# Kernel optimization log

Measured on AMD Instinct MI355X. Metric: run time of the kernel, lower is better.

Reference implementation:

```python
import jax, jax.numpy as jnp
import numpy as np

WIN = (8, 7, 7)
N_TOK = WIN[0] * WIN[1] * WIN[2]  # 392
DIM = 128
N_HEADS = 4
TABLE = (2 * WIN[0] - 1) * (2 * WIN[1] - 1) * (2 * WIN[2] - 1)  # 2535


def _relative_position_index():
    # Faithful port of the torch buffer construction in __init__.
    coords = np.stack(np.meshgrid(np.arange(WIN[0]), np.arange(WIN[1]), np.arange(WIN[2]), indexing='ij'))
    flat = coords.reshape(3, -1)                       # (3, N)
    rel = flat[:, :, None] - flat[:, None, :]          # (3, N, N)
    rel = rel.transpose(1, 2, 0).astype(np.int64)      # (N, N, 3)
    rel[..., 0] += WIN[0] - 1
    rel[..., 1] += WIN[1] - 1
    rel[..., 2] += WIN[2] - 1
    rel[..., 0] *= (2 * WIN[1] - 1) * (2 * WIN[2] - 1)
    rel[..., 1] *= 2 * WIN[2] - 1
    return rel.sum(-1)                                 # (N, N)


def setup_inputs() -> dict:
    key = jax.random.key(0)
    k1, k2, k3, k4 = jax.random.split(key, 4)
    B_ = 256   # B=1 batch * 256 windows of a 32x224x224 clip (D=32,H=56,W=56)
    nW = 256
    x = jax.random.normal(k1, (B_, N_TOK, DIM), dtype=jnp.float32)
    mask = jnp.zeros((nW, N_TOK, N_TOK), dtype=jnp.float32)  # 0/-inf shift mask; non-shift -> zeros
    bias_table = 0.02 * jax.random.normal(k2, (TABLE, N_HEADS), dtype=jnp.float32)
    rel_index = jnp.asarray(_relative_position_index(), dtype=jnp.int32)
    qkv_w = 0.02 * jax.random.normal(k3, (3 * DIM, DIM), dtype=jnp.float32)
    proj_w = 0.02 * jax.random.normal(k4, (DIM, DIM), dtype=jnp.float32)
    proj_b = jnp.zeros((DIM,), dtype=jnp.float32)
    return {"x": x, "mask": mask, "bias_table": bias_table, "rel_index": rel_index,
            "qkv_w": qkv_w, "proj_w": proj_w, "proj_b": proj_b}


def reference(x, mask, bias_table, rel_index, qkv_w, proj_w, proj_b):
    B_, N, C = x.shape
    nH = N_HEADS
    hd = C // nH
    scale = hd ** -0.5
    # qkv projection (no bias), split heads -> (3, B_, nH, N, hd)
    qkv = (x @ qkv_w.T).reshape(B_, N, 3, nH, hd).transpose(2, 0, 3, 1, 4)
    q, k, v = qkv[0], qkv[1], qkv[2]
    # relative position bias: gather table -> (nH, N, N)
    bias = bias_table[rel_index.reshape(-1)].reshape(N, N, nH).transpose(2, 0, 1)
    # scores: (B_, nH, N, N)
    attn = jnp.einsum('bhnd,bhmd->bhnm', q * scale, k) + bias[None]
    nW = mask.shape[0]
    attn = attn.reshape(B_ // nW, nW, nH, N, N) + mask[None, :, None]
    attn = jax.nn.softmax(attn.reshape(B_, nH, N, N), axis=-1)
    y = jnp.einsum('bhnm,bhmd->bhnd', attn, v)            # (B_, nH, N, hd)
    y = y.transpose(0, 2, 1, 3).reshape(B_, N, C)
    return y @ proj_w.T + proj_b
```

## Files before the change

### kernel.cpp

```cpp
#include <hip/hip_runtime.h>
#include <hip/hip_bf16.h>
#include <stdint.h>

#define NTOK 392
#define DIM  128
#define NH   4
#define HD   32
#define NCH  13
#define KST  36
#define VST  396
#define L2E  1.44269504f
#define BPQ  416

typedef __attribute__((ext_vector_type(4))) float f32x4;
typedef __attribute__((ext_vector_type(4))) short s16x4;
typedef __attribute__((ext_vector_type(8))) short s16x8;

union Frag { s16x8 v; struct { s16x4 lo, hi; } h; };
union PF { s16x8 v; uint32_t u[4]; };

__device__ __forceinline__ short f2bf(float f) {
  union { float f; uint32_t u; } v; v.f = f;
  uint32_t r = v.u + 0x7fffu + ((v.u >> 16) & 1u);
  return (short)(r >> 16);
}
__device__ __forceinline__ s16x4 cvt4(f32x4 a) {
  s16x4 r; r.x = f2bf(a.x); r.y = f2bf(a.y); r.z = f2bf(a.z); r.w = f2bf(a.w);
  return r;
}
__device__ __forceinline__ float fexp2(float x) {
  float r; asm("v_exp_f32 %0, %1" : "=v"(r) : "v"(x)); return r;
}
__device__ __forceinline__ void bb2f(s16x8 b, f32x4& lo, f32x4& hi) {
  union { s16x8 s; uint32_t u[4]; } x; x.s = b;
  union { uint32_t u; float f; } t;
  t.u = x.u[0] << 16;          lo.x = t.f;
  t.u = x.u[0] & 0xffff0000u;  lo.y = t.f;
  t.u = x.u[1] << 16;          lo.z = t.f;
  t.u = x.u[1] & 0xffff0000u;  lo.w = t.f;
  t.u = x.u[2] << 16;          hi.x = t.f;
  t.u = x.u[2] & 0xffff0000u;  hi.y = t.f;
  t.u = x.u[3] << 16;          hi.z = t.f;
  t.u = x.u[3] & 0xffff0000u;  hi.w = t.f;
}

__device__ __forceinline__ void sm_pv(f32x4 s0, f32x4 s1,
                                      f32x4& o0, f32x4& o1,
                                      float& mrun, float& nmrl, float& lrun,
                                      const Frag& vf0, const Frag& vf1) {
  float cm = fmaxf(fmaxf(fmaxf(s0.x, s0.y), fmaxf(s0.z, s0.w)),
                   fmaxf(fmaxf(s1.x, s1.y), fmaxf(s1.z, s1.w)));
  if (__any(cm > mrun + 8.f)) {
    float tmx = fmaxf(cm, __shfl_xor(cm, 16));
    tmx = fmaxf(tmx, __shfl_xor(tmx, 32));
    const float mnew = fmaxf(mrun, tmx);
    const float al = fexp2((mrun - mnew) * L2E);
    #pragma unroll
    for (int rr = 0; rr < 4; ++rr) { o0[rr] *= al; o1[rr] *= al; }
    lrun *= al; mrun = mnew; nmrl = -mnew * L2E;
  }
  float p0 = fexp2(fmaf(s0.x, L2E, nmrl));
  float p1 = fexp2(fmaf(s0.y, L2E, nmrl));
  float p2 = fexp2(fmaf(s0.z, L2E, nmrl));
  float p3 = fexp2(fmaf(s0.w, L2E, nmrl));
  float p4 = fexp2(fmaf(s1.x, L2E, nmrl));
  float p5 = fexp2(fmaf(s1.y, L2E, nmrl));
  float p6 = fexp2(fmaf(s1.z, L2E, nmrl));
  float p7 = fexp2(fmaf(s1.w, L2E, nmrl));
  lrun += ((p0 + p1) + (p2 + p3)) + ((p4 + p5) + (p6 + p7));
  PF pf;
  asm("v_cvt_pk_bf16_f32 %0, %1, %2" : "=v"(pf.u[0]) : "v"(p0), "v"(p1));
  asm("v_cvt_pk_bf16_f32 %0, %1, %2" : "=v"(pf.u[1]) : "v"(p2), "v"(p3));
  asm("v_cvt_pk_bf16_f32 %0, %1, %2" : "=v"(pf.u[2]) : "v"(p4), "v"(p5));
  asm("v_cvt_pk_bf16_f32 %0, %1, %2" : "=v"(pf.u[3]) : "v"(p6), "v"(p7));
  o0 = __builtin_amdgcn_mfma_f32_16x16x32_bf16(vf0.v, pf.v, o0, 0, 0, 0);
  o1 = __builtin_amdgcn_mfma_f32_16x16x32_bf16(vf1.v, pf.v, o1, 0, 0, 0);
}

__global__ void k_biasperm(const float* __restrict__ bt, const int* __restrict__ ri,
                           short* __restrict__ bias_perm) {
  int i = blockIdx.x * 256 + threadIdx.x;
  if (i >= NH * NTOK * BPQ) return;
  int h = i / (NTOK * BPQ);
  int r = i - h * (NTOK * BPQ);
  int q = r / BPQ;
  int p = r - q * BPQ;
  int c = p >> 5, w2 = p & 31;
  int g = w2 >> 3, hb = (w2 >> 2) & 1, jj = w2 & 3;
  int kv = c * 32 + hb * 16 + g * 4 + jj;
  float v = -3e30f;
  if (kv < NTOK) v = bt[ri[q * NTOK + kv] * NH + h];
  bias_perm[i] = f2bf(v);
}

__global__ void k_wprep(const float* __restrict__ qkvw, const float* __restrict__ pw,
                        short* __restrict__ wq_bf, short* __restrict__ wp_bf) {
  int i = blockIdx.x * 256 + threadIdx.x;
  if (i < 3 * DIM * DIM) wq_bf[i] = f2bf(qkvw[i]);
  if (i < DIM * DIM)     wp_bf[i] = f2bf(pw[i]);
}

__global__ __launch_bounds__(256, 2)
void k_qkv(const float* __restrict__ x, const short* __restrict__ wq_bf,
           short* __restrict__ q_ws, short* __restrict__ k_ws,
           short* __restrict__ v_ws) {
  __shared__ short xs[64 * 136];
  __shared__ short wl[128 * 136];
  const int t  = threadIdx.x;
  const int m0 = blockIdx.x * 64;
  {
    const int r = t >> 2, c0 = (t & 3) * 32;
    const float* src = x + (size_t)(m0 + r) * DIM + c0;
    short* dst = xs + r * 136 + c0;
    #pragma unroll
    for (int i = 0; i < 8; ++i)
      *(s16x4*)(dst + 4*i) = cvt4(*(const f32x4*)(src + 4*i));
  }
  const int l = t & 63, w = t >> 6, lr = l & 15, g = l >> 4;
  const int m = m0 + w * 16 + lr;
  const int b = m / NTOK;
  const int n = m - b * NTOK;
  #pragma unroll 1
  for (int z = 0; z < 3; ++z) {
    {
      const int r = t >> 1, c0 = (t & 1) * 64;
      const short* src = wq_bf + (size_t)(z * DIM + r) * DIM + c0;
      short* dst = wl + r * 136 + c0;
      #pragma unroll
      for (int i = 0; i < 8; ++i)
        *(s16x8*)(dst + 8*i) = *(const s16x8*)(src + 8*i);
    }
    __syncthreads();
    f32x4 acc[8] = {};
    #pragma unroll
    for (int ks = 0; ks < 4; ++ks) {
      const int k0 = ks * 32 + 4 * g;
      Frag xb;
      const short* bp = xs + (w * 16 + lr) * 136 + k0;
      xb.h.lo = *(const s16x4*)bp; xb.h.hi = *(const s16x4*)(bp + 16);
      #pragma unroll
      for (int ct = 0; ct < 8; ++ct) {
        const short* ap = wl + (ct * 16 + lr) * 136 + k0;
        Frag wa; wa.h.lo = *(const s16x4*)ap; wa.h.hi = *(const s16x4*)(ap + 16);
        acc[ct] = __builtin_amdgcn_mfma_f32_16x16x32_bf16(wa.v, xb.v, acc[ct], 0, 0, 0);
      }
    }
    short* outp = (z == 0) ? q_ws : (z == 1 ? k_ws : v_ws);
    const float scale = (z == 0) ? 0.17677669529663689f : 1.0f;
    #pragma unroll
    for (int ct = 0; ct < 8; ++ct) {
      const int c0 = ct * 16 + 4 * g;
      const int hh = c0 >> 5, d = c0 & 31;
      f32x4 sc = acc[ct];
      sc.x *= scale; sc.y *= scale; sc.z *= scale; sc.w *= scale;
      *(s16x4*)(outp + (((size_t)b * NH + hh) * NTOK + n) * HD + d) = cvt4(sc);
    }
    __syncthreads();
  }
}

__global__ __launch_bounds__(512, 4)
void k_attn(const short* __restrict__ q_ws, const short* __restrict__ k_ws,
            const short* __restrict__ v_ws, const float* __restrict__ mask,
            const short* __restrict__ bias_perm, short* __restrict__ y_ws) {
  __shared__ short K_l[NTOK * KST];
  __shared__ short Vt[HD * VST];
  const int t = threadIdx.x;
  const int j = blockIdx.x, xcd = j & 7, slot = j >> 3;
  const int b = (xcd << 5) | (slot >> 2);
  const int h = slot & 3;
  const size_t bh = (size_t)b * NH + h;
  const short* kp = k_ws + bh * NTOK * HD;
  const short* vp = v_ws + bh * NTOK * HD;
  const short* qp = q_ws + bh * NTOK * HD;
  const float* mp = mask + (size_t)b * NTOK * NTOK;
  const short* bph = bias_perm + (size_t)h * NTOK * BPQ;
  for (int r = t; r < NTOK; r += 512) {
    short* dst = K_l + r * KST;
    const s16x4* src = (const s16x4*)(kp + r * HD);
    #pragma unroll
    for (int i = 0; i < 8; ++i) *(s16x4*)(dst + 4*i) = src[i];
  }
  for (int n = t; n < NTOK; n += 512) {
    union { s16x4 v4[8]; short s[32]; } vv;
    const s16x4* src = (const s16x4*)(vp + n * HD);
    #pragma unroll
    for (int i = 0; i < 8; ++i) vv.v4[i] = src[i];
    #pragma unroll
    for (int d = 0; d < 32; ++d) Vt[d * VST + n] = vv.s[d];
  }
  __syncthreads();
  const int l = t & 63, w = t >> 6, lr = l & 15, g = l >> 4;
  const int og0 = 4 * g, og1 = 16 + 4 * g;
  #pragma unroll 1
  for (int q0 = w * 16; q0 < NTOK; q0 += 128) {
    const int qrow = q0 + lr;
    const int qc = qrow < NTOK ? qrow : NTOK - 1;
    Frag qf;
    { const short* qa = qp + qc * HD + 4 * g;
      qf.h.lo = *(const s16x4*)qa; qf.h.hi = *(const s16x4*)(qa + 16); }
    const float* mrow = mp + (size_t)qc * NTOK;
    const short* brow = bph + qc * BPQ;
    f32x4 mm0[5], mm1[5];
    s16x8 bb[5];
    #pragma unroll
    for (int c = 0; c < 4; ++c) {
      mm0[c] = *(const f32x4*)(mrow + c * 32 + og0);
      mm1[c] = *(const f32x4*)(mrow + c * 32 + og1);
      bb[c]  = *(const s16x8*)(brow + c * 32 + g * 8);
    }
    f32x4 o0 = {0,0,0,0}, o1 = {0,0,0,0};
    float mrun = 0.f, nmrl = 0.f, lrun = 0.f;
    #pragma unroll
    for (int c = 0; c < NCH; ++c) {
      const int sl = c % 5;
      if (c + 4 < NCH) {
        const int cc = c + 4, s2 = (c + 4) % 5;
        int a0 = cc * 32 + og0, a1 = cc * 32 + og1;
        if (cc == NCH - 1) { a0 = a0 > 388 ? 388 : a0; a1 = 388; }
        mm0[s2] = *(const f32x4*)(mrow + a0);
        mm1[s2] = *(const f32x4*)(mrow + a1);
        bb[s2]  = *(const s16x8*)(brow + cc * 32 + g * 8);
      }
      const int kv0 = c * 32;
      int r0 = kv0 + lr, r1 = kv0 + 16 + lr;
      int cb0 = kv0 + 4 * g, cb1 = kv0 + 16 + 4 * g;
      if (c == NCH - 1) {
        r0 = r0 < NTOK ? r0 : NTOK - 1;
        r1 = NTOK - 1;
        cb0 = cb0 < 388 ? cb0 : 388;
        cb1 = 388;
      }
      Frag ka0, ka1, vf0, vf1;
      { const short* p0 = K_l + r0 * KST + 4 * g;
        ka0.h.lo = *(const s16x4*)p0; ka0.h.hi = *(const s16x4*)(p0 + 16);
        const short* p1 = K_l + r1 * KST + 4 * g;
        ka1.h.lo = *(const s16x4*)p1; ka1.h.hi = *(const s16x4*)(p1 + 16);
        const short* v0 = Vt + lr * VST;
        vf0.h.lo = *(const s16x4*)(v0 + cb0); vf0.h.hi = *(const s16x4*)(v0 + cb1);
        const short* v1 = Vt + (16 + lr) * VST;
        vf1.h.lo = *(const s16x4*)(v1 + cb0); vf1.h.hi = *(const s16x4*)(v1 + cb1); }
      f32x4 blo, bhi;
      bb2f(bb[sl], blo, bhi);
      f32x4 c0 = mm0[sl] + blo;
      f32x4 c1 = mm1[sl] + bhi;
      __builtin_amdgcn_s_setprio(1);
      f32x4 s0 = __builtin_amdgcn_mfma_f32_16x16x32_bf16(ka0.v, qf.v, c0, 0,0,0);
      f32x4 s1 = __builtin_amdgcn_mfma_f32_16x16x32_bf16(ka1.v, qf.v, c1, 0,0,0);
      sm_pv(s0, s1, o0, o1, mrun, nmrl, lrun, vf0, vf1);
      __builtin_amdgcn_s_setprio(0);
    }
    float lt = lrun + __shfl_xor(lrun, 16);
    lt += __shfl_xor(lt, 32);
    if (qrow < NTOK) {
      const float inv = 1.0f / lt;
      short* yb = y_ws + ((size_t)b * NTOK + qrow) * DIM + h * HD;
      s16x4 r0v, r1v;
      #pragma unroll
      for (int rr = 0; rr < 4; ++rr) { r0v[rr] = f2bf(o0[rr] * inv); r1v[rr] = f2bf(o1[rr] * inv); }
      *(s16x4*)(yb + 4 * g) = r0v;
      *(s16x4*)(yb + 16 + 4 * g) = r1v;
    }
  }
}

__global__ __launch_bounds__(256, 2)
void k_proj(const short* __restrict__ y_ws, const short* __restrict__ wp_bf,
            const float* __restrict__ pb, float* __restrict__ out) {
  __shared__ short ys[64 * 136];
  __shared__ short wl[128 * 136];
  const int t = threadIdx.x;
  const int m0 = blockIdx.x * 64;
  {
    const int r = t >> 2, c0 = (t & 3) * 32;
    const s16x4* src = (const s16x4*)(y_ws + (size_t)(m0 + r) * DIM + c0);
    short* dst = ys + r * 136 + c0;
    #pragma unroll
    for (int i = 0; i < 8; ++i) *(s16x4*)(dst + 4*i) = src[i];
  }
  {
    const int r = t >> 1, c0 = (t & 1) * 64;
    const short* src = wp_bf + (size_t)r * DIM + c0;
    short* dst = wl + r * 136 + c0;
    #pragma unroll
    for (int i = 0; i < 8; ++i)
      *(s16x8*)(dst + 8*i) = *(const s16x8*)(src + 8*i);
  }
  __syncthreads();
  const int l = t & 63, w = t >> 6, lr = l & 15, g = l >> 4;
  const int m = m0 + w * 16 + lr;
  f32x4 acc[8] = {};
  #pragma unroll
  for (int ks = 0; ks < 4; ++ks) {
    const int k0 = ks * 32 + 4 * g;
    Frag ya;
    const short* bp = ys + (w * 16 + lr) * 136 + k0;
    ya.h.lo = *(const s16x4*)bp; ya.h.hi = *(const s16x4*)(bp + 16);
    #pragma unroll
    for (int ct = 0; ct < 8; ++ct) {
      const short* ap = wl + (ct * 16 + lr) * 136 + k0;
      Frag wa; wa.h.lo = *(const s16x4*)ap; wa.h.hi = *(const s16x4*)(ap + 16);
      acc[ct] = __builtin_amdgcn_mfma_f32_16x16x32_bf16(wa.v, ya.v, acc[ct], 0, 0, 0);
    }
  }
  #pragma unroll
  for (int ct = 0; ct < 8; ++ct) {
    const int c0 = ct * 16 + 4 * g;
    const f32x4 pbv = *(const f32x4*)(pb + c0);
    f32x4 res = acc[ct] + pbv;
    *(f32x4*)(out + (size_t)m * DIM + c0) = res;
  }
}

extern "C" void kernel_launch(void* const* d_in, const int* in_sizes, int n_in,
                              void* d_out, int out_size, void* d_ws, size_t ws_size,
                              hipStream_t stream) {
  const float* x    = (const float*)d_in[0];
  const float* mask = (const float*)d_in[1];
  const float* bt   = (const float*)d_in[2];
  const int*   ri   = (const int*)d_in[3];
  const float* qkvw = (const float*)d_in[4];
  const float* pw   = (const float*)d_in[5];
  const float* pb   = (const float*)d_in[6];
  float* out = (float*)d_out;
  const size_t TEN = (size_t)256 * NH * NTOK * HD;
  short* q_ws = (short*)d_ws;
  short* k_ws = q_ws + TEN;
  short* v_ws = k_ws + TEN;
  short* y_ws = v_ws + TEN;
  short* bias_perm = y_ws + TEN;
  short* wq_bf = bias_perm + (size_t)NH * NTOK * BPQ;
  short* wp_bf = wq_bf + 3 * DIM * DIM;
  k_biasperm<<<(NH * NTOK * BPQ + 255) / 256, 256, 0, stream>>>(bt, ri, bias_perm);
  k_wprep<<<(3 * DIM * DIM + 255) / 256, 256, 0, stream>>>(qkvw, pw, wq_bf, wp_bf);
  k_qkv<<<1568, 256, 0, stream>>>(x, wq_bf, q_ws, k_ws, v_ws);
  k_attn<<<1024, 512, 0, stream>>>(q_ws, k_ws, v_ws, mask, bias_perm, y_ws);
  k_proj<<<1568, 256, 0, stream>>>(y_ws, wp_bf, pb, out);
}
```

Before: 214.3 us.

## Process two query tiles per wave in attention, merge prep kernels, tweak launch bounds

The attention kernel now has each wave handle two 16-row query tiles at once, with 25 tiles split over two passes. This reuses each K and V LDS fragment load for both tiles, and the mask/bias prefetch depth is cut from 4 chunks to a double buffer. The bias-permutation and weight-conversion kernels are merged into one launch, and cvt4 uses the packed bf16 convert instruction. Launch bounds change (attn 4→2 blocks, qkv/proj 2→3), trading occupancy for more registers and shallower prefetch, which may expose global load latency.

```diff
diff --git a/kernel.cpp b/kernel.cpp
--- a/kernel.cpp
+++ b/kernel.cpp
@@ -25,8 +25,10 @@
   return (short)(r >> 16);
 }
 __device__ __forceinline__ s16x4 cvt4(f32x4 a) {
-  s16x4 r; r.x = f2bf(a.x); r.y = f2bf(a.y); r.z = f2bf(a.z); r.w = f2bf(a.w);
-  return r;
+  union { s16x4 s; uint32_t u[2]; } r;
+  asm("v_cvt_pk_bf16_f32 %0, %1, %2" : "=v"(r.u[0]) : "v"(a.x), "v"(a.y));
+  asm("v_cvt_pk_bf16_f32 %0, %1, %2" : "=v"(r.u[1]) : "v"(a.z), "v"(a.w));
+  return r.s;
 }
 __device__ __forceinline__ float fexp2(float x) {
   float r; asm("v_exp_f32 %0, %1" : "=v"(r) : "v"(x)); return r;
@@ -77,9 +79,13 @@
   o1 = __builtin_amdgcn_mfma_f32_16x16x32_bf16(vf1.v, pf.v, o1, 0, 0, 0);
 }
 
-__global__ void k_biasperm(const float* __restrict__ bt, const int* __restrict__ ri,
-                           short* __restrict__ bias_perm) {
+__global__ void k_prep(const float* __restrict__ bt, const int* __restrict__ ri,
+                       short* __restrict__ bias_perm,
+                       const float* __restrict__ qkvw, const float* __restrict__ pw,
+                       short* __restrict__ wq_bf, short* __restrict__ wp_bf) {
   int i = blockIdx.x * 256 + threadIdx.x;
+  if (i < 3 * DIM * DIM) wq_bf[i] = f2bf(qkvw[i]);
+  if (i < DIM * DIM)     wp_bf[i] = f2bf(pw[i]);
   if (i >= NH * NTOK * BPQ) return;
   int h = i / (NTOK * BPQ);
   int r = i - h * (NTOK * BPQ);
@@ -93,14 +99,7 @@
   bias_perm[i] = f2bf(v);
 }
 
-__global__ void k_wprep(const float* __restrict__ qkvw, const float* __restrict__ pw,
-                        short* __restrict__ wq_bf, short* __restrict__ wp_bf) {
-  int i = blockIdx.x * 256 + threadIdx.x;
-  if (i < 3 * DIM * DIM) wq_bf[i] = f2bf(qkvw[i]);
-  if (i < DIM * DIM)     wp_bf[i] = f2bf(pw[i]);
-}
-
-__global__ __launch_bounds__(256, 2)
+__global__ __launch_bounds__(256, 3)
 void k_qkv(const float* __restrict__ x, const short* __restrict__ wq_bf,
            short* __restrict__ q_ws, short* __restrict__ k_ws,
            short* __restrict__ v_ws) {
@@ -159,7 +158,7 @@
   }
 }
 
-__global__ __launch_bounds__(512, 4)
+__global__ __launch_bounds__(512, 2)
 void k_attn(const short* __restrict__ q_ws, const short* __restrict__ k_ws,
             const short* __restrict__ v_ws, const float* __restrict__ mask,
             const short* __restrict__ bias_perm, short* __restrict__ y_ws) {
@@ -193,34 +192,60 @@
   const int l = t & 63, w = t >> 6, lr = l & 15, g = l >> 4;
   const int og0 = 4 * g, og1 = 16 + 4 * g;
   #pragma unroll 1
-  for (int q0 = w * 16; q0 < NTOK; q0 += 128) {
-    const int qrow = q0 + lr;
-    const int qc = qrow < NTOK ? qrow : NTOK - 1;
-    Frag qf;
-    { const short* qa = qp + qc * HD + 4 * g;
-      qf.h.lo = *(const s16x4*)qa; qf.h.hi = *(const s16x4*)(qa + 16); }
-    const float* mrow = mp + (size_t)qc * NTOK;
-    const short* brow = bph + qc * BPQ;
-    f32x4 mm0[5], mm1[5];
-    s16x8 bb[5];
-    #pragma unroll
-    for (int c = 0; c < 4; ++c) {
-      mm0[c] = *(const f32x4*)(mrow + c * 32 + og0);
-      mm1[c] = *(const f32x4*)(mrow + c * 32 + og1);
-      bb[c]  = *(const s16x8*)(brow + c * 32 + g * 8);
-    }
-    f32x4 o0 = {0,0,0,0}, o1 = {0,0,0,0};
-    float mrun = 0.f, nmrl = 0.f, lrun = 0.f;
+  for (int pass = 0; pass < 2; ++pass) {
+    const int T0 = w + pass * 16, T1 = T0 + 8;
+    const bool do1 = (T1 < 25);
+    const int qrowA = T0 * 16 + lr;
+    const int qrowB = T1 * 16 + lr;
+    const int qcB = qrowB < NTOK ? qrowB : NTOK - 1;
+    Frag qfA, qfB;
+    { const short* qa = qp + qrowA * HD + 4 * g;
+      qfA.h.lo = *(const s16x4*)qa; qfA.h.hi = *(const s16x4*)(qa + 16); }
+    { const short* qa = qp + qcB * HD + 4 * g;
+      qfB.h.lo = *(const s16x4*)qa; qfB.h.hi = *(const s16x4*)(qa + 16); }
+    const float* mrowA = mp + (size_t)qrowA * NTOK;
+    const short* browA = bph + qrowA * BPQ;
+    const float* mrowB = mp + (size_t)qcB * NTOK;
+    const short* browB = bph + qcB * BPQ;
+    f32x4 maf0[2], maf1[2], mbf0[2], mbf1[2];
+    s16x8 baf[2], bbf[2];
+    maf0[0] = *(const f32x4*)(mrowA + og0);
+    maf1[0] = *(const f32x4*)(mrowA + og1);
+    baf[0]  = *(const s16x8*)(browA + g * 8);
+    if (do1) {
+      mbf0[0] = *(const f32x4*)(mrowB + og0);
+      mbf1[0] = *(const f32x4*)(mrowB + og1);
+      bbf[0]  = *(const s16x8*)(browB + g * 8);
+    }
+    f32x4 oA0 = {0,0,0,0}, oA1 = {0,0,0,0}, oB0 = {0,0,0,0}, oB1 = {0,0,0,0};
+    float mrunA = 0.f, nmrlA = 0.f, lrunA = 0.f;
+    float mrunB = 0.f, nmrlB = 0.f, lrunB = 0.f;
     #pragma unroll
     for (int c = 0; c < NCH; ++c) {
-      const int sl = c % 5;
-      if (c + 4 < NCH) {
-        const int cc = c + 4, s2 = (c + 4) % 5;
-        int a0 = cc * 32 + og0, a1 = cc * 32 + og1;
-        if (cc == NCH - 1) { a0 = a0 > 388 ? 388 : a0; a1 = 388; }
-        mm0[s2] = *(const f32x4*)(mrow + a0);
-        mm1[s2] = *(const f32x4*)(mrow + a1);
-        bb[s2]  = *(const s16x8*)(brow + cc * 32 + g * 8);
+      const int sl = c & 1, nx = sl ^ 1;
+      if (c < NCH - 1) {
+        const int cc = c + 1;
+        if (cc < NCH - 1) {
+          const int base = cc * 32;
+          maf0[nx] = *(const f32x4*)(mrowA + base + og0);
+          maf1[nx] = *(const f32x4*)(mrowA + base + og1);
+          baf[nx]  = *(const s16x8*)(browA + base + g * 8);
+          if (do1) {
+            mbf0[nx] = *(const f32x4*)(mrowB + base + og0);
+            mbf1[nx] = *(const f32x4*)(mrowB + base + og1);
+            bbf[nx]  = *(const s16x8*)(browB + base + g * 8);
+          }
+        } else {
+          int a0 = 384 + og0; if (a0 > 388) a0 = 388;
+          maf0[nx] = *(const f32x4*)(mrowA + a0);
+          maf1[nx] = *(const f32x4*)(mrowA + 388);
+          baf[nx]  = *(const s16x8*)(browA + 384 + g * 8);
+          if (do1) {
+            mbf0[nx] = *(const f32x4*)(mrowB + a0);
+            mbf1[nx] = *(const f32x4*)(mrowB + 388);
+            bbf[nx]  = *(const s16x8*)(browB + 384 + g * 8);
+          }
+        }
       }
       const int kv0 = c * 32;
       int r0 = kv0 + lr, r1 = kv0 + 16 + lr;
@@ -240,31 +265,54 @@
         vf0.h.lo = *(const s16x4*)(v0 + cb0); vf0.h.hi = *(const s16x4*)(v0 + cb1);
         const short* v1 = Vt + (16 + lr) * VST;
         vf1.h.lo = *(const s16x4*)(v1 + cb0); vf1.h.hi = *(const s16x4*)(v1 + cb1); }
-      f32x4 blo, bhi;
-      bb2f(bb[sl], blo, bhi);
-      f32x4 c0 = mm0[sl] + blo;
-      f32x4 c1 = mm1[sl] + bhi;
       __builtin_amdgcn_s_setprio(1);
-      f32x4 s0 = __builtin_amdgcn_mfma_f32_16x16x32_bf16(ka0.v, qf.v, c0, 0,0,0);
-      f32x4 s1 = __builtin_amdgcn_mfma_f32_16x16x32_bf16(ka1.v, qf.v, c1, 0,0,0);
-      sm_pv(s0, s1, o0, o1, mrun, nmrl, lrun, vf0, vf1);
+      { f32x4 aL, aH;
+        bb2f(baf[sl], aL, aH);
+        f32x4 c0 = maf0[sl] + aL;
+        f32x4 c1 = maf1[sl] + aH;
+        f32x4 s0 = __builtin_amdgcn_mfma_f32_16x16x32_bf16(ka0.v, qfA.v, c0, 0,0,0);
+        f32x4 s1 = __builtin_amdgcn_mfma_f32_16x16x32_bf16(ka1.v, qfA.v, c1, 0,0,0);
+        sm_pv(s0, s1, oA0, oA1, mrunA, nmrlA, lrunA, vf0, vf1);
+      }
+      if (do1) {
+        f32x4 bL, bH;
+        bb2f(bbf[sl], bL, bH);
+        f32x4 c0 = mbf0[sl] + bL;
+        f32x4 c1 = mbf1[sl] + bH;
+        f32x4 s0 = __builtin_amdgcn_mfma_f32_16x16x32_bf16(ka0.v, qfB.v, c0, 0,0,0);
+        f32x4 s1 = __builtin_amdgcn_mfma_f32_16x16x32_bf16(ka1.v, qfB.v, c1, 0,0,0);
+        sm_pv(s0, s1, oB0, oB1, mrunB, nmrlB, lrunB, vf0, vf1);
+      }
       __builtin_amdgcn_s_setprio(0);
     }
-    float lt = lrun + __shfl_xor(lrun, 16);
-    lt += __shfl_xor(lt, 32);
-    if (qrow < NTOK) {
+    {
+      float lt = lrunA + __shfl_xor(lrunA, 16);
+      lt += __shfl_xor(lt, 32);
       const float inv = 1.0f / lt;
-      short* yb = y_ws + ((size_t)b * NTOK + qrow) * DIM + h * HD;
+      short* yb = y_ws + ((size_t)b * NTOK + qrowA) * DIM + h * HD;
       s16x4 r0v, r1v;
       #pragma unroll
-      for (int rr = 0; rr < 4; ++rr) { r0v[rr] = f2bf(o0[rr] * inv); r1v[rr] = f2bf(o1[rr] * inv); }
+      for (int rr = 0; rr < 4; ++rr) { r0v[rr] = f2bf(oA0[rr] * inv); r1v[rr] = f2bf(oA1[rr] * inv); }
       *(s16x4*)(yb + 4 * g) = r0v;
       *(s16x4*)(yb + 16 + 4 * g) = r1v;
     }
-  }
-}
-
-__global__ __launch_bounds__(256, 2)
+    if (do1) {
+      float lt = lrunB + __shfl_xor(lrunB, 16);
+      lt += __shfl_xor(lt, 32);
+      if (qrowB < NTOK) {
+        const float inv = 1.0f / lt;
+        short* yb = y_ws + ((size_t)b * NTOK + qrowB) * DIM + h * HD;
+        s16x4 r0v, r1v;
+        #pragma unroll
+        for (int rr = 0; rr < 4; ++rr) { r0v[rr] = f2bf(oB0[rr] * inv); r1v[rr] = f2bf(oB1[rr] * inv); }
+        *(s16x4*)(yb + 4 * g) = r0v;
+        *(s16x4*)(yb + 16 + 4 * g) = r1v;
+      }
+    }
+  }
+}
+
+__global__ __launch_bounds__(256, 3)
 void k_proj(const short* __restrict__ y_ws, const short* __restrict__ wp_bf,
             const float* __restrict__ pb, float* __restrict__ out) {
   __shared__ short ys[64 * 136];
@@ -331,8 +379,8 @@
   short* bias_perm = y_ws + TEN;
   short* wq_bf = bias_perm + (size_t)NH * NTOK * BPQ;
   short* wp_bf = wq_bf + 3 * DIM * DIM;
-  k_biasperm<<<(NH * NTOK * BPQ + 255) / 256, 256, 0, stream>>>(bt, ri, bias_perm);
-  k_wprep<<<(3 * DIM * DIM + 255) / 256, 256, 0, stream>>>(qkvw, pw, wq_bf, wp_bf);
+  k_prep<<<(NH * NTOK * BPQ + 255) / 256, 256, 0, stream>>>(bt, ri, bias_perm,
+                                                            qkvw, pw, wq_bf, wp_bf);
   k_qkv<<<1568, 256, 0, stream>>>(x, wq_bf, q_ws, k_ws, v_ws);
   k_attn<<<1024, 512, 0, stream>>>(q_ws, k_ws, v_ws, mask, bias_perm, y_ws);
   k_proj<<<1568, 256, 0, stream>>>(y_ws, wp_bf, pb, out);
```

Measured after the change: 225.1 us. 5.0% more time.
